# Kernel tuning notes

Hardware: AMD Instinct MI355X
Metric: run time of the kernel (lower is better)

Reference implementation:

```python
import jax, jax.numpy as jnp
import numpy as np
from jax import lax

EPS = 1e-8
TAU = 1.0  # step=0 < tau_warmup_steps -> tau = tau_init


def setup_inputs() -> dict:
    key = jax.random.key(0)
    k1, k2 = jax.random.split(key)
    B, D, H, W = 4, 256, 32, 32
    C, K, d = 8, 1024, 32  # n_codebooks, vocab_size, codebook_dim (D = C*d)
    z = jax.random.normal(k1, (B, D, H, W), dtype=jnp.float32)
    cb = jax.random.normal(k2, (C, K, d), dtype=jnp.float32)
    cb = cb / (jnp.linalg.norm(cb, axis=-1, keepdims=True) + 1e-12) * np.sqrt(d).astype(np.float32)
    return {"z": z, "codebooks": cb}


def reference(z, codebooks):
    # Training-mode forward of LGQuantizer (step=0).
    B, D, H, W = z.shape
    C, K, d = codebooks.shape
    # (b d h w) -> (b h w) (c d_sub): chunk along channel dim
    zf = z.transpose(0, 2, 3, 1).reshape(-1, C, d)  # [N, C, d]
    N = zf.shape[0]

    # pairwise squared distances per codebook: [N, C, K]
    z_sq = jnp.sum(zf * zf, axis=-1)                      # [N, C]
    cb_sq = jnp.sum(codebooks * codebooks, axis=-1)       # [C, K]
    cross = jnp.einsum('ncd,ckd->nck', zf, codebooks)     # [N, C, K]
    dists = z_sq[:, :, None] - 2.0 * cross + cb_sq[None, :, :]

    inv_temp = 1.0 / (2.0 * TAU * TAU + EPS)
    logits = -dists * inv_temp
    q = jax.nn.softmax(logits, axis=-1)                   # [N, C, K]

    # soft quantization + straight-through with hard lookup
    z_q = jnp.einsum('nck,ckd->ncd', q, codebooks)        # [N, C, d]
    idx = jnp.argmin(dists, axis=-1)                      # [N, C]
    z_q_hard = codebooks[jnp.arange(C)[None, :], idx]     # [N, C, d]
    z_q_st = z_q + lax.stop_gradient(z_q_hard - z_q)

    quantized = z_q_st.reshape(B, H, W, D).transpose(0, 3, 1, 2)  # [B, D, H, W]
    indices = idx.reshape(B, H, W, C).transpose(0, 3, 1, 2)       # [B, C, H, W]

    # commitment: mse(z_part, q.detach() @ cb.detach()), averaged over codebooks
    commitment = jnp.mean((zf - lax.stop_gradient(z_q)) ** 2)

    log_q = jnp.log(q + EPS)
    neg_ent = jnp.sum(q * log_q, axis=-1)                 # [N, C]
    expected_dist = jnp.mean(jnp.sum(q * dists, axis=-1), axis=0)  # [C]
    kl_uniform = jnp.mean(neg_ent, axis=0) + np.log(K).astype(np.float32)  # [C]
    free_energy = jnp.mean(expected_dist * inv_temp + kl_uniform)

    confidence_loss = jnp.mean(-neg_ent)

    q_bar = jnp.mean(q, axis=0)                           # [C, K]
    balance_loss = jnp.mean(jnp.sum(q_bar * jnp.log(q_bar * K + EPS), axis=-1))

    return (quantized, indices, q, commitment, free_energy,
            confidence_loss, balance_loss, jnp.float32(TAU))
```

## Files before the change

### kernel.cpp

```cpp
#include <hip/hip_runtime.h>

#define WS_A0 0
#define WS_A1 1
#define WS_A2 2
#define WS_QBAR 16
#define WS_CBSQ (WS_QBAR + 8192)
#define WS_IDX  (WS_CBSQ + 8192)

#define OUT_IDX  1048576
#define OUT_Q    1081344
#define OUT_SCAL 34635776

__device__ __forceinline__ float wsum64(float v) {
#pragma unroll
  for (int m = 32; m >= 1; m >>= 1) v += __shfl_xor(v, m, 64);
  return v;
}

__device__ __forceinline__ float uread(float v) {
  return __int_as_float(__builtin_amdgcn_readfirstlane(__float_as_int(v)));
}

#define ZLD 33
__global__ __launch_bounds__(1024, 4)
void k_main(
    const float* __restrict__ z, const float* __restrict__ cb,
    float* __restrict__ out, float* __restrict__ ws_f, int* __restrict__ ws_i) {
  __shared__ __attribute__((aligned(16))) float smem[39040];
  float* cb_lds   = smem;
  float* qsum     = smem + 32768;
  float* cbsq_lds = smem + 33792;
  float* z_lds    = smem + 34816;

  const int c    = blockIdx.x >> 5;
  const int nblk = blockIdx.x & 31;
  const int tid  = threadIdx.x;
  const int lane = tid & 63;
  const int wave = tid >> 6;

  const int bb   = (nblk * 128) >> 10;
  const int hwb  = (nblk * 128) & 1023;

  const float4* cb4 = (const float4*)(cb + (size_t)c * 32768);
  float4* lds4 = (float4*)cb_lds;
#pragma unroll
  for (int i = 0; i < 8; ++i) {
    int idx = i * 1024 + tid;
    int k = idx >> 3, q = idx & 7;
    lds4[(k << 3) + (q ^ (k & 7))] = cb4[idx];
  }
  qsum[tid] = 0.f;
  {
    const float* zbase = z + (((size_t)bb * 256 + c * 32) << 10) + hwb;
#pragma unroll
    for (int i = 0; i < 4; ++i) {
      int idx = i * 1024 + tid;
      int d = idx >> 7, j = idx & 127;
      z_lds[j * ZLD + d] = zbase[(size_t)d * 1024 + j];
    }
  }
  __syncthreads();
  {
    float s = 0.f;
    const int t7 = tid & 7;
#pragma unroll
    for (int q = 0; q < 8; ++q) {
      float4 r4 = lds4[(tid << 3) + (q ^ t7)];
      s = fmaf(r4.x, r4.x, s); s = fmaf(r4.y, r4.y, s);
      s = fmaf(r4.z, r4.z, s); s = fmaf(r4.w, r4.w, s);
    }
    cbsq_lds[tid] = s;
  }
  __syncthreads();

  float* out_q   = out + OUT_Q;
  float* out_idx = out + OUT_IDX;

  float accA1 = 0.f, accA2 = 0.f;
  float a0loc = 0.f;
  const int kl7 = lane & 7;

#pragma unroll 1
  for (int pp = 0; pp < 4; ++pp) {
    const int nl0 = wave * 8 + pp * 2;
    const int nl1 = nl0 + 1;
    const int n0 = nblk * 128 + nl0;
    const int n1 = n0 + 1;

    float zv0[32], zv1[32];
#pragma unroll
    for (int d = 0; d < 32; ++d) {
      zv0[d] = uread(z_lds[nl0 * ZLD + d]);
      zv1[d] = uread(z_lds[nl1 * ZLD + d]);
    }
    float zs0 = 0.f, zs1 = 0.f;
#pragma unroll
    for (int d = 0; d < 32; ++d) {
      zs0 = fmaf(zv0[d], zv0[d], zs0);
      zs1 = fmaf(zv1[d], zv1[d], zs1);
    }

    float S0 = 0.f, S1 = 0.f, es0 = 0.f, es1 = 0.f;
    float zqA0[16], zqA1[16];
#pragma unroll
    for (int i = 0; i < 16; ++i) { zqA0[i] = 0.f; zqA1[i] = 0.f; }

#pragma unroll 1
    for (int jj = 0; jj < 16; ++jj) {
      const int k = jj * 64 + lane;
      const int kbase = k << 3;
      float cq = cbsq_lds[k];
      float a0 = 0.f, a1 = 0.f, g0 = 0.f, g1 = 0.f;
#pragma unroll
      for (int qq = 0; qq < 6; ++qq) {
        const int q = (qq + 4) & 7;
        float4 r4 = lds4[kbase + (q ^ kl7)];
        a0 = fmaf(r4.x, zv0[q * 4 + 0], a0);
        a1 = fmaf(r4.y, zv0[q * 4 + 1], a1);
        a0 = fmaf(r4.z, zv0[q * 4 + 2], a0);
        a1 = fmaf(r4.w, zv0[q * 4 + 3], a1);
        g0 = fmaf(r4.x, zv1[q * 4 + 0], g0);
        g1 = fmaf(r4.y, zv1[q * 4 + 1], g1);
        g0 = fmaf(r4.z, zv1[q * 4 + 2], g0);
        g1 = fmaf(r4.w, zv1[q * 4 + 3], g1);
      }
      float4 kq2 = lds4[kbase + (2 ^ kl7)];
      a0 = fmaf(kq2.x, zv0[8], a0);  a1 = fmaf(kq2.y, zv0[9], a1);
      a0 = fmaf(kq2.z, zv0[10], a0); a1 = fmaf(kq2.w, zv0[11], a1);
      g0 = fmaf(kq2.x, zv1[8], g0);  g1 = fmaf(kq2.y, zv1[9], g1);
      g0 = fmaf(kq2.z, zv1[10], g0); g1 = fmaf(kq2.w, zv1[11], g1);
      float4 kq3 = lds4[kbase + (3 ^ kl7)];
      a0 = fmaf(kq3.x, zv0[12], a0); a1 = fmaf(kq3.y, zv0[13], a1);
      a0 = fmaf(kq3.z, zv0[14], a0); a1 = fmaf(kq3.w, zv0[15], a1);
      g0 = fmaf(kq3.x, zv1[12], g0); g1 = fmaf(kq3.y, zv1[13], g1);
      g0 = fmaf(kq3.z, zv1[14], g0); g1 = fmaf(kq3.w, zv1[15], g1);

      float s0 = (a0 + a1) - 0.5f * cq;
      float s1 = (g0 + g1) - 0.5f * cq;
      float ev0 = __expf(s0), ev1 = __expf(s1);
      S0 += ev0;  S1 += ev1;
      es0 = fmaf(ev0, s0, es0);
      es1 = fmaf(ev1, s1, es1);
#pragma unroll
      for (int q = 0; q < 2; ++q) {
        float4 r4 = lds4[kbase + (q ^ kl7)];
        zqA0[q * 4 + 0] = fmaf(ev0, r4.x, zqA0[q * 4 + 0]);
        zqA0[q * 4 + 1] = fmaf(ev0, r4.y, zqA0[q * 4 + 1]);
        zqA0[q * 4 + 2] = fmaf(ev0, r4.z, zqA0[q * 4 + 2]);
        zqA0[q * 4 + 3] = fmaf(ev0, r4.w, zqA0[q * 4 + 3]);
        zqA1[q * 4 + 0] = fmaf(ev1, r4.x, zqA1[q * 4 + 0]);
        zqA1[q * 4 + 1] = fmaf(ev1, r4.y, zqA1[q * 4 + 1]);
        zqA1[q * 4 + 2] = fmaf(ev1, r4.z, zqA1[q * 4 + 2]);
        zqA1[q * 4 + 3] = fmaf(ev1, r4.w, zqA1[q * 4 + 3]);
      }
      zqA0[8]  = fmaf(ev0, kq2.x, zqA0[8]);  zqA0[9]  = fmaf(ev0, kq2.y, zqA0[9]);
      zqA0[10] = fmaf(ev0, kq2.z, zqA0[10]); zqA0[11] = fmaf(ev0, kq2.w, zqA0[11]);
      zqA1[8]  = fmaf(ev1, kq2.x, zqA1[8]);  zqA1[9]  = fmaf(ev1, kq2.y, zqA1[9]);
      zqA1[10] = fmaf(ev1, kq2.z, zqA1[10]); zqA1[11] = fmaf(ev1, kq2.w, zqA1[11]);
      zqA0[12] = fmaf(ev0, kq3.x, zqA0[12]); zqA0[13] = fmaf(ev0, kq3.y, zqA0[13]);
      zqA0[14] = fmaf(ev0, kq3.z, zqA0[14]); zqA0[15] = fmaf(ev0, kq3.w, zqA0[15]);
      zqA1[12] = fmaf(ev1, kq3.x, zqA1[12]); zqA1[13] = fmaf(ev1, kq3.y, zqA1[13]);
      zqA1[14] = fmaf(ev1, kq3.z, zqA1[14]); zqA1[15] = fmaf(ev1, kq3.w, zqA1[15]);
    }

    float St0 = wsum64(S0), St1 = wsum64(S1);
    float rS0 = 1.f / St0, rS1 = 1.f / St1;
    float est0 = wsum64(es0), est1 = wsum64(es1);

    accA1 += (zs0 - 2.f * est0 * rS0) + (zs1 - 2.f * est1 * rS1);
    accA2 += (est0 * rS0 - __logf(St0)) + (est1 * rS1 - __logf(St1));

    {
#pragma unroll
      for (int t = 0; t < 4; ++t) {
        const int half = 8 >> t;
        const int up = (lane >> (5 - t)) & 1;
#pragma unroll
        for (int i = 0; i < half; ++i) {
          float sa0 = up ? zqA0[i] : zqA0[i + half];
          float ka0 = up ? zqA0[i + half] : zqA0[i];
          zqA0[i] = ka0 + __shfl_xor(sa0, 32 >> t, 64);
          float sa1 = up ? zqA1[i] : zqA1[i + half];
          float ka1 = up ? zqA1[i + half] : zqA1[i];
          zqA1[i] = ka1 + __shfl_xor(sa1, 32 >> t, 64);
        }
      }
      zqA0[0] += __shfl_xor(zqA0[0], 2, 64);
      zqA0[0] += __shfl_xor(zqA0[0], 1, 64);
      zqA1[0] += __shfl_xor(zqA1[0], 2, 64);
      zqA1[0] += __shfl_xor(zqA1[0], 1, 64);
      const int ddA = (lane >> 2) & 15;
      float dA0 = z_lds[nl0 * ZLD + ddA] - zqA0[0] * rS0;
      float dA1 = z_lds[nl1 * ZLD + ddA] - zqA1[0] * rS1;
      a0loc += dA0 * dA0 + dA1 * dA1;
    }

    float sm0 = -INFINITY, sm1 = -INFINITY;
    int km0 = 0, km1 = 0;
    float zqB0[16], zqB1[16];
#pragma unroll
    for (int i = 0; i < 16; ++i) { zqB0[i] = 0.f; zqB1[i] = 0.f; }
    float* qp0 = out_q + ((size_t)n0 * 8 + c) * 1024;
    float* qp1 = out_q + ((size_t)n1 * 8 + c) * 1024;

#pragma unroll 1
    for (int jj = 0; jj < 16; ++jj) {
      const int k = jj * 64 + lane;
      const int kbase = k << 3;
      float cq = cbsq_lds[k];
      float a0 = 0.f, a1 = 0.f, g0 = 0.f, g1 = 0.f;
#pragma unroll
      for (int q = 0; q < 4; ++q) {
        float4 r4 = lds4[kbase + (q ^ kl7)];
        a0 = fmaf(r4.x, zv0[q * 4 + 0], a0);
        a1 = fmaf(r4.y, zv0[q * 4 + 1], a1);
        a0 = fmaf(r4.z, zv0[q * 4 + 2], a0);
        a1 = fmaf(r4.w, zv0[q * 4 + 3], a1);
        g0 = fmaf(r4.x, zv1[q * 4 + 0], g0);
        g1 = fmaf(r4.y, zv1[q * 4 + 1], g1);
        g0 = fmaf(r4.z, zv1[q * 4 + 2], g0);
        g1 = fmaf(r4.w, zv1[q * 4 + 3], g1);
      }
      float4 kq4 = lds4[kbase + (4 ^ kl7)];
      a0 = fmaf(kq4.x, zv0[16], a0); a1 = fmaf(kq4.y, zv0[17], a1);
      a0 = fmaf(kq4.z, zv0[18], a0); a1 = fmaf(kq4.w, zv0[19], a1);
      g0 = fmaf(kq4.x, zv1[16], g0); g1 = fmaf(kq4.y, zv1[17], g1);
      g0 = fmaf(kq4.z, zv1[18], g0); g1 = fmaf(kq4.w, zv1[19], g1);
      float4 kq5 = lds4[kbase + (5 ^ kl7)];
      a0 = fmaf(kq5.x, zv0[20], a0); a1 = fmaf(kq5.y, zv0[21], a1);
      a0 = fmaf(kq5.z, zv0[22], a0); a1 = fmaf(kq5.w, zv0[23], a1);
      g0 = fmaf(kq5.x, zv1[20], g0); g1 = fmaf(kq5.y, zv1[21], g1);
      g0 = fmaf(kq5.z, zv1[22], g0); g1 = fmaf(kq5.w, zv1[23], g1);
      float4 kq6 = lds4[kbase + (6 ^ kl7)];
      a0 = fmaf(kq6.x, zv0[24], a0); a1 = fmaf(kq6.y, zv0[25], a1);
      a0 = fmaf(kq6.z, zv0[26], a0); a1 = fmaf(kq6.w, zv0[27], a1);
      g0 = fmaf(kq6.x, zv1[24], g0); g1 = fmaf(kq6.y, zv1[25], g1);
      g0 = fmaf(kq6.z, zv1[26], g0); g1 = fmaf(kq6.w, zv1[27], g1);
      float4 kq7 = lds4[kbase + (7 ^ kl7)];
      a0 = fmaf(kq7.x, zv0[28], a0); a1 = fmaf(kq7.y, zv0[29], a1);
      a0 = fmaf(kq7.z, zv0[30], a0); a1 = fmaf(kq7.w, zv0[31], a1);
      g0 = fmaf(kq7.x, zv1[28], g0); g1 = fmaf(kq7.y, zv1[29], g1);
      g0 = fmaf(kq7.z, zv1[30], g0); g1 = fmaf(kq7.w, zv1[31], g1);

      float s0 = (a0 + a1) - 0.5f * cq;
      float s1 = (g0 + g1) - 0.5f * cq;
      if (s0 > sm0) { sm0 = s0; km0 = k; }
      if (s1 > sm1) { sm1 = s1; km1 = k; }
      float qv0 = __expf(s0) * rS0;
      float qv1 = __expf(s1) * rS1;
      __builtin_nontemporal_store(qv0, qp0 + jj * 64 + lane);
      __builtin_nontemporal_store(qv1, qp1 + jj * 64 + lane);
      atomicAdd(&qsum[jj * 64 + lane], qv0 + qv1);
      zqB0[0]  = fmaf(qv0, kq4.x, zqB0[0]);  zqB0[1]  = fmaf(qv0, kq4.y, zqB0[1]);
      zqB0[2]  = fmaf(qv0, kq4.z, zqB0[2]);  zqB0[3]  = fmaf(qv0, kq4.w, zqB0[3]);
      zqB1[0]  = fmaf(qv1, kq4.x, zqB1[0]);  zqB1[1]  = fmaf(qv1, kq4.y, zqB1[1]);
      zqB1[2]  = fmaf(qv1, kq4.z, zqB1[2]);  zqB1[3]  = fmaf(qv1, kq4.w, zqB1[3]);
      zqB0[4]  = fmaf(qv0, kq5.x, zqB0[4]);  zqB0[5]  = fmaf(qv0, kq5.y, zqB0[5]);
      zqB0[6]  = fmaf(qv0, kq5.z, zqB0[6]);  zqB0[7]  = fmaf(qv0, kq5.w, zqB0[7]);
      zqB1[4]  = fmaf(qv1, kq5.x, zqB1[4]);  zqB1[5]  = fmaf(qv1, kq5.y, zqB1[5]);
      zqB1[6]  = fmaf(qv1, kq5.z, zqB1[6]);  zqB1[7]  = fmaf(qv1, kq5.w, zqB1[7]);
      zqB0[8]  = fmaf(qv0, kq6.x, zqB0[8]);  zqB0[9]  = fmaf(qv0, kq6.y, zqB0[9]);
      zqB0[10] = fmaf(qv0, kq6.z, zqB0[10]); zqB0[11] = fmaf(qv0, kq6.w, zqB0[11]);
      zqB1[8]  = fmaf(qv1, kq6.x, zqB1[8]);  zqB1[9]  = fmaf(qv1, kq6.y, zqB1[9]);
      zqB1[10] = fmaf(qv1, kq6.z, zqB1[10]); zqB1[11] = fmaf(qv1, kq6.w, zqB1[11]);
      zqB0[12] = fmaf(qv0, kq7.x, zqB0[12]); zqB0[13] = fmaf(qv0, kq7.y, zqB0[13]);
      zqB0[14] = fmaf(qv0, kq7.z, zqB0[14]); zqB0[15] = fmaf(qv0, kq7.w, zqB0[15]);
      zqB1[12] = fmaf(qv1, kq7.x, zqB1[12]); zqB1[13] = fmaf(qv1, kq7.y, zqB1[13]);
      zqB1[14] = fmaf(qv1, kq7.z, zqB1[14]); zqB1[15] = fmaf(qv1, kq7.w, zqB1[15]);
    }

#pragma unroll
    for (int m = 32; m >= 1; m >>= 1) {
      float so = __shfl_xor(sm0, m, 64); int ko = __shfl_xor(km0, m, 64);
      if (so > sm0 || (so == sm0 && ko < km0)) { sm0 = so; km0 = ko; }
      float sp = __shfl_xor(sm1, m, 64); int kp = __shfl_xor(km1, m, 64);
      if (sp > sm1 || (sp == sm1 && kp < km1)) { sm1 = sp; km1 = kp; }
    }
    if (lane == 0) {
      out_idx[(size_t)bb * 8192 + c * 1024 + hwb + nl0] = (float)km0;
      ws_i[WS_IDX + n0 * 8 + c] = km0;
      out_idx[(size_t)bb * 8192 + c * 1024 + hwb + nl1] = (float)km1;
      ws_i[WS_IDX + n1 * 8 + c] = km1;
    }

#pragma unroll
    for (int t = 0; t < 4; ++t) {
      const int half = 8 >> t;
      const int up = (lane >> (5 - t)) & 1;
#pragma unroll
      for (int i = 0; i < half; ++i) {
        float sa0 = up ? zqB0[i] : zqB0[i + half];
        float ka0 = up ? zqB0[i + half] : zqB0[i];
        zqB0[i] = ka0 + __shfl_xor(sa0, 32 >> t, 64);
        float sa1 = up ? zqB1[i] : zqB1[i + half];
        float ka1 = up ? zqB1[i + half] : zqB1[i];
        zqB1[i] = ka1 + __shfl_xor(sa1, 32 >> t, 64);
      }
    }
    zqB0[0] += __shfl_xor(zqB0[0], 2, 64);
    zqB0[0] += __shfl_xor(zqB0[0], 1, 64);
    zqB1[0] += __shfl_xor(zqB1[0], 2, 64);
    zqB1[0] += __shfl_xor(zqB1[0], 1, 64);
    const int ddB = (lane >> 2) & 15;
    float dB0 = z_lds[nl0 * ZLD + 16 + ddB] - zqB0[0];
    float dB1 = z_lds[nl1 * ZLD + 16 + ddB] - zqB1[0];
    a0loc += dB0 * dB0 + dB1 * dB1;
  }

  float accA0 = 0.25f * wsum64(a0loc);
  if (lane == 0) {
    atomicAdd(&ws_f[WS_A0], accA0);
    atomicAdd(&ws_f[WS_A1], accA1);
    atomicAdd(&ws_f[WS_A2], accA2);
  }

  __syncthreads();
  atomicAdd(&ws_f[WS_QBAR + c * 1024 + tid], qsum[tid]);
}

__global__ __launch_bounds__(256) void k_hard(const float* __restrict__ cb,
                                              const int* __restrict__ ws_i,
                                              float* __restrict__ out0,
                                              const float* __restrict__ ws_f,
                                              float* __restrict__ out_s) {
  int o4 = blockIdx.x * 256 + threadIdx.x;
  int o  = o4 << 2;
  int b  = o >> 18;
  int r  = o & 262143;
  int ch = r >> 10;
  int hw = r & 1023;
  int c = ch >> 5, dd = ch & 31;
  int n = (b << 10) + hw;
  const int* ip = ws_i + WS_IDX + n * 8 + c;
  const float* cbc = cb + ((size_t)c << 15) + dd;
  float4 v;
  v.x = cbc[(size_t)ip[0]  * 32];
  v.y = cbc[(size_t)ip[8]  * 32];
  v.z = cbc[(size_t)ip[16] * 32];
  v.w = cbc[(size_t)ip[24] * 32];
  *(float4*)(out0 + o) = v;

  if (blockIdx.x == 0) {
    __shared__ float red[256];
    int tid = threadIdx.x;
    float bal = 0.f;
    for (int i = tid; i < 8192; i += 256) {
      float qb = ws_f[WS_QBAR + i] * (1.0f / 4096.0f);
      bal += qb * __logf(qb * 1024.0f + 1e-8f);
    }
    red[tid] = bal;
    __syncthreads();
    for (int s = 128; s > 0; s >>= 1) {
      if (tid < s) red[tid] += red[tid + s];
      __syncthreads();
    }
    if (tid == 0) {
      float A0 = ws_f[WS_A0], A1 = ws_f[WS_A1], A2 = ws_f[WS_A2];
      out_s[0] = A0 * (1.0f / 1048576.0f);
      out_s[1] = (0.5f * A1 + A2) * (1.0f / 32768.0f) + 6.93147180559945f;
      out_s[2] = -A2 * (1.0f / 32768.0f);
      out_s[3] = red[0] * 0.125f;
      out_s[4] = 1.0f;
    }
  }
}

extern "C" void kernel_launch(void* const* d_in, const int* in_sizes, int n_in,
                              void* d_out, int out_size, void* d_ws, size_t ws_size,
                              hipStream_t stream) {
  (void)in_sizes; (void)n_in; (void)out_size; (void)ws_size;
  const float* z  = (const float*)d_in[0];
  const float* cb = (const float*)d_in[1];
  float* out  = (float*)d_out;
  float* ws_f = (float*)d_ws;
  int*   ws_i = (int*)d_ws;

  hipMemsetAsync(d_ws, 0, (WS_QBAR + 8192) * sizeof(float), stream);
  k_main <<<256, 1024, 0, stream>>>(z, cb, out, ws_f, ws_i);
  k_hard <<<1024, 256, 0, stream>>>(cb, ws_i, out, ws_f, out + OUT_SCAL);
}
```

Baseline: 436.4 us.

## Fuse hard codebook lookup into main kernel using LDS-resident codebook

Moves the hard-quantized output gather from a separate kernel into the end of the main kernel. It keeps the argmin indices in shared memory and reads codeword values from the codebook tile already in LDS, which removes the global index round trip and the gather kernel's scattered global reads. The scalar-loss reductions are deferred: per-lane partial sums replace two wave reductions per point pair, and the loss kernel shrinks to a single-block finalizer. The score loop is also restructured to reuse the first two codeword float4 loads for the soft accumulation instead of reloading them.

New measurement: 408.3 us. 1.07x faster.

```diff
diff --git a/kernel.cpp b/kernel.cpp
--- a/kernel.cpp
+++ b/kernel.cpp
@@ -4,8 +4,6 @@
 #define WS_A1 1
 #define WS_A2 2
 #define WS_QBAR 16
-#define WS_CBSQ (WS_QBAR + 8192)
-#define WS_IDX  (WS_CBSQ + 8192)
 
 #define OUT_IDX  1048576
 #define OUT_Q    1081344
@@ -25,8 +23,9 @@
 __global__ __launch_bounds__(1024, 4)
 void k_main(
     const float* __restrict__ z, const float* __restrict__ cb,
-    float* __restrict__ out, float* __restrict__ ws_f, int* __restrict__ ws_i) {
+    float* __restrict__ out, float* __restrict__ ws_f) {
   __shared__ __attribute__((aligned(16))) float smem[39040];
+  __shared__ int km_lds[128];
   float* cb_lds   = smem;
   float* qsum     = smem + 32768;
   float* cbsq_lds = smem + 33792;
@@ -76,7 +75,9 @@
   float* out_q   = out + OUT_Q;
   float* out_idx = out + OUT_IDX;
 
-  float accA1 = 0.f, accA2 = 0.f;
+  float zsum = 0.f;
+  float logsum = 0.f;
+  float a12loc = 0.f;
   float a0loc = 0.f;
   const int kl7 = lane & 7;
 
@@ -99,6 +100,7 @@
       zs0 = fmaf(zv0[d], zv0[d], zs0);
       zs1 = fmaf(zv1[d], zv1[d], zs1);
     }
+    zsum += zs0 + zs1;
 
     float S0 = 0.f, S1 = 0.f, es0 = 0.f, es1 = 0.f;
     float zqA0[16], zqA1[16];
@@ -112,8 +114,7 @@
       float cq = cbsq_lds[k];
       float a0 = 0.f, a1 = 0.f, g0 = 0.f, g1 = 0.f;
 #pragma unroll
-      for (int qq = 0; qq < 6; ++qq) {
-        const int q = (qq + 4) & 7;
+      for (int q = 4; q < 8; ++q) {
         float4 r4 = lds4[kbase + (q ^ kl7)];
         a0 = fmaf(r4.x, zv0[q * 4 + 0], a0);
         a1 = fmaf(r4.y, zv0[q * 4 + 1], a1);
@@ -124,6 +125,16 @@
         g0 = fmaf(r4.z, zv1[q * 4 + 2], g0);
         g1 = fmaf(r4.w, zv1[q * 4 + 3], g1);
       }
+      float4 kq0 = lds4[kbase + (0 ^ kl7)];
+      a0 = fmaf(kq0.x, zv0[0], a0);  a1 = fmaf(kq0.y, zv0[1], a1);
+      a0 = fmaf(kq0.z, zv0[2], a0);  a1 = fmaf(kq0.w, zv0[3], a1);
+      g0 = fmaf(kq0.x, zv1[0], g0);  g1 = fmaf(kq0.y, zv1[1], g1);
+      g0 = fmaf(kq0.z, zv1[2], g0);  g1 = fmaf(kq0.w, zv1[3], g1);
+      float4 kq1 = lds4[kbase + (1 ^ kl7)];
+      a0 = fmaf(kq1.x, zv0[4], a0);  a1 = fmaf(kq1.y, zv0[5], a1);
+      a0 = fmaf(kq1.z, zv0[6], a0);  a1 = fmaf(kq1.w, zv0[7], a1);
+      g0 = fmaf(kq1.x, zv1[4], g0);  g1 = fmaf(kq1.y, zv1[5], g1);
+      g0 = fmaf(kq1.z, zv1[6], g0);  g1 = fmaf(kq1.w, zv1[7], g1);
       float4 kq2 = lds4[kbase + (2 ^ kl7)];
       a0 = fmaf(kq2.x, zv0[8], a0);  a1 = fmaf(kq2.y, zv0[9], a1);
       a0 = fmaf(kq2.z, zv0[10], a0); a1 = fmaf(kq2.w, zv0[11], a1);
@@ -141,18 +152,14 @@
       S0 += ev0;  S1 += ev1;
       es0 = fmaf(ev0, s0, es0);
       es1 = fmaf(ev1, s1, es1);
-#pragma unroll
-      for (int q = 0; q < 2; ++q) {
-        float4 r4 = lds4[kbase + (q ^ kl7)];
-        zqA0[q * 4 + 0] = fmaf(ev0, r4.x, zqA0[q * 4 + 0]);
-        zqA0[q * 4 + 1] = fmaf(ev0, r4.y, zqA0[q * 4 + 1]);
-        zqA0[q * 4 + 2] = fmaf(ev0, r4.z, zqA0[q * 4 + 2]);
-        zqA0[q * 4 + 3] = fmaf(ev0, r4.w, zqA0[q * 4 + 3]);
-        zqA1[q * 4 + 0] = fmaf(ev1, r4.x, zqA1[q * 4 + 0]);
-        zqA1[q * 4 + 1] = fmaf(ev1, r4.y, zqA1[q * 4 + 1]);
-        zqA1[q * 4 + 2] = fmaf(ev1, r4.z, zqA1[q * 4 + 2]);
-        zqA1[q * 4 + 3] = fmaf(ev1, r4.w, zqA1[q * 4 + 3]);
-      }
+      zqA0[0]  = fmaf(ev0, kq0.x, zqA0[0]);  zqA0[1]  = fmaf(ev0, kq0.y, zqA0[1]);
+      zqA0[2]  = fmaf(ev0, kq0.z, zqA0[2]);  zqA0[3]  = fmaf(ev0, kq0.w, zqA0[3]);
+      zqA1[0]  = fmaf(ev1, kq0.x, zqA1[0]);  zqA1[1]  = fmaf(ev1, kq0.y, zqA1[1]);
+      zqA1[2]  = fmaf(ev1, kq0.z, zqA1[2]);  zqA1[3]  = fmaf(ev1, kq0.w, zqA1[3]);
+      zqA0[4]  = fmaf(ev0, kq1.x, zqA0[4]);  zqA0[5]  = fmaf(ev0, kq1.y, zqA0[5]);
+      zqA0[6]  = fmaf(ev0, kq1.z, zqA0[6]);  zqA0[7]  = fmaf(ev0, kq1.w, zqA0[7]);
+      zqA1[4]  = fmaf(ev1, kq1.x, zqA1[4]);  zqA1[5]  = fmaf(ev1, kq1.y, zqA1[5]);
+      zqA1[6]  = fmaf(ev1, kq1.z, zqA1[6]);  zqA1[7]  = fmaf(ev1, kq1.w, zqA1[7]);
       zqA0[8]  = fmaf(ev0, kq2.x, zqA0[8]);  zqA0[9]  = fmaf(ev0, kq2.y, zqA0[9]);
       zqA0[10] = fmaf(ev0, kq2.z, zqA0[10]); zqA0[11] = fmaf(ev0, kq2.w, zqA0[11]);
       zqA1[8]  = fmaf(ev1, kq2.x, zqA1[8]);  zqA1[9]  = fmaf(ev1, kq2.y, zqA1[9]);
@@ -165,10 +172,8 @@
 
     float St0 = wsum64(S0), St1 = wsum64(S1);
     float rS0 = 1.f / St0, rS1 = 1.f / St1;
-    float est0 = wsum64(es0), est1 = wsum64(es1);
-
-    accA1 += (zs0 - 2.f * est0 * rS0) + (zs1 - 2.f * est1 * rS1);
-    accA2 += (est0 * rS0 - __logf(St0)) + (est1 * rS1 - __logf(St1));
+    a12loc += es0 * rS0 + es1 * rS1;
+    logsum += __logf(St0) + __logf(St1);
 
     {
 #pragma unroll
@@ -278,9 +283,9 @@
     }
     if (lane == 0) {
       out_idx[(size_t)bb * 8192 + c * 1024 + hwb + nl0] = (float)km0;
-      ws_i[WS_IDX + n0 * 8 + c] = km0;
       out_idx[(size_t)bb * 8192 + c * 1024 + hwb + nl1] = (float)km1;
-      ws_i[WS_IDX + n1 * 8 + c] = km1;
+      km_lds[nl0] = km0;
+      km_lds[nl1] = km1;
     }
 
 #pragma unroll
@@ -308,60 +313,49 @@
   }
 
   float accA0 = 0.25f * wsum64(a0loc);
+  float E = wsum64(a12loc);
   if (lane == 0) {
     atomicAdd(&ws_f[WS_A0], accA0);
-    atomicAdd(&ws_f[WS_A1], accA1);
-    atomicAdd(&ws_f[WS_A2], accA2);
+    atomicAdd(&ws_f[WS_A1], zsum - 2.f * E);
+    atomicAdd(&ws_f[WS_A2], E - logsum);
   }
 
   __syncthreads();
   atomicAdd(&ws_f[WS_QBAR + c * 1024 + tid], qsum[tid]);
-}
-
-__global__ __launch_bounds__(256) void k_hard(const float* __restrict__ cb,
-                                              const int* __restrict__ ws_i,
-                                              float* __restrict__ out0,
-                                              const float* __restrict__ ws_f,
-                                              float* __restrict__ out_s) {
-  int o4 = blockIdx.x * 256 + threadIdx.x;
-  int o  = o4 << 2;
-  int b  = o >> 18;
-  int r  = o & 262143;
-  int ch = r >> 10;
-  int hw = r & 1023;
-  int c = ch >> 5, dd = ch & 31;
-  int n = (b << 10) + hw;
-  const int* ip = ws_i + WS_IDX + n * 8 + c;
-  const float* cbc = cb + ((size_t)c << 15) + dd;
-  float4 v;
-  v.x = cbc[(size_t)ip[0]  * 32];
-  v.y = cbc[(size_t)ip[8]  * 32];
-  v.z = cbc[(size_t)ip[16] * 32];
-  v.w = cbc[(size_t)ip[24] * 32];
-  *(float4*)(out0 + o) = v;
-
-  if (blockIdx.x == 0) {
-    __shared__ float red[256];
-    int tid = threadIdx.x;
-    float bal = 0.f;
-    for (int i = tid; i < 8192; i += 256) {
-      float qb = ws_f[WS_QBAR + i] * (1.0f / 4096.0f);
-      bal += qb * __logf(qb * 1024.0f + 1e-8f);
-    }
-    red[tid] = bal;
+
+#pragma unroll
+  for (int i = 0; i < 4; ++i) {
+    int idx = i * 1024 + tid;
+    int dd = idx >> 7, nl = idx & 127;
+    int km = km_lds[nl];
+    int slot = (dd >> 2) ^ (km & 7);
+    float v = cb_lds[((km << 3) + slot) * 4 + (dd & 3)];
+    out[(((size_t)bb * 256 + c * 32 + dd) << 10) + hwb + nl] = v;
+  }
+}
+
+__global__ __launch_bounds__(256) void k_final(const float* __restrict__ ws_f,
+                                               float* __restrict__ out_s) {
+  __shared__ float red[256];
+  int tid = threadIdx.x;
+  float bal = 0.f;
+  for (int i = tid; i < 8192; i += 256) {
+    float qb = ws_f[WS_QBAR + i] * (1.0f / 4096.0f);
+    bal += qb * __logf(qb * 1024.0f + 1e-8f);
+  }
+  red[tid] = bal;
+  __syncthreads();
+  for (int s = 128; s > 0; s >>= 1) {
+    if (tid < s) red[tid] += red[tid + s];
     __syncthreads();
-    for (int s = 128; s > 0; s >>= 1) {
-      if (tid < s) red[tid] += red[tid + s];
-      __syncthreads();
-    }
-    if (tid == 0) {
-      float A0 = ws_f[WS_A0], A1 = ws_f[WS_A1], A2 = ws_f[WS_A2];
-      out_s[0] = A0 * (1.0f / 1048576.0f);
-      out_s[1] = (0.5f * A1 + A2) * (1.0f / 32768.0f) + 6.93147180559945f;
-      out_s[2] = -A2 * (1.0f / 32768.0f);
-      out_s[3] = red[0] * 0.125f;
-      out_s[4] = 1.0f;
-    }
+  }
+  if (tid == 0) {
+    float A0 = ws_f[WS_A0], A1 = ws_f[WS_A1], A2 = ws_f[WS_A2];
+    out_s[0] = A0 * (1.0f / 1048576.0f);
+    out_s[1] = (0.5f * A1 + A2) * (1.0f / 32768.0f) + 6.93147180559945f;
+    out_s[2] = -A2 * (1.0f / 32768.0f);
+    out_s[3] = red[0] * 0.125f;
+    out_s[4] = 1.0f;
   }
 }
 
@@ -373,9 +367,8 @@
   const float* cb = (const float*)d_in[1];
   float* out  = (float*)d_out;
   float* ws_f = (float*)d_ws;
-  int*   ws_i = (int*)d_ws;
 
   hipMemsetAsync(d_ws, 0, (WS_QBAR + 8192) * sizeof(float), stream);
-  k_main <<<256, 1024, 0, stream>>>(z, cb, out, ws_f, ws_i);
-  k_hard <<<1024, 256, 0, stream>>>(cb, ws_i, out, ws_f, out + OUT_SCAL);
-}
+  k_main <<<256, 1024, 0, stream>>>(z, cb, out, ws_f);
+  k_final<<<1,    256, 0, stream>>>(ws_f, out + OUT_SCAL);
+}
```
